# Performance work log

Measured on AMD Instinct MI355X. Metric: run time of the kernel, lower is better.

The kernel has to match this reference:

```python
import jax, jax.numpy as jnp
import numpy as np

N = 60000      # nodes in batch (max_num_cg_nodes_in_batch = 80000)
E = 150000     # edges per edge type
T = 4          # primary edge types (doubled by add_backwards_edges -> 8)
D = 64         # hidden / embedding size
V = 10000      # subtoken vocab
S = 5          # max subtokens per node label
TIMESTEPS = [7, 1]


def setup_inputs() -> dict:
    key = jax.random.key(0)
    ks = jax.random.split(key, 12)
    sc = 1.0 / np.sqrt(D)
    return {
        "node_subtokens": jax.random.randint(ks[0], (N, S), 0, V),
        "adjacency_lists": jax.random.randint(ks[1], (T, E, 2), 0, N),
        "embed_table": jax.random.normal(ks[2], (V, D), jnp.float32) * 0.1,
        "proj_W": jax.random.normal(ks[3], (D, D), jnp.float32) * sc,
        "edge_W0": jax.random.normal(ks[4], (2 * T, D, D), jnp.float32) * sc,
        "edge_W1": jax.random.normal(ks[5], (2 * T, D, D), jnp.float32) * sc,
        "gru0_Wx": jax.random.normal(ks[6], (D, 3 * D), jnp.float32) * sc,
        "gru0_Wh": jax.random.normal(ks[7], (D, 3 * D), jnp.float32) * sc,
        "gru0_b": jnp.zeros((3 * D,), jnp.float32),
        "gru1_Wx": jax.random.normal(ks[8], (2 * D, 3 * D), jnp.float32) * sc,
        "gru1_Wh": jax.random.normal(ks[9], (D, 3 * D), jnp.float32) * sc,
        "gru1_b": jnp.zeros((3 * D,), jnp.float32),
    }


def _gru(x, h, Wx, Wh, b):
    gx = x @ Wx + b          # [N, 3D]
    gh = h @ Wh              # [N, 3D]
    xr, xu, xc = jnp.split(gx, 3, axis=-1)
    hr, hu, hc = jnp.split(gh, 3, axis=-1)
    r = jax.nn.sigmoid(xr + hr)
    u = jax.nn.sigmoid(xu + hu)
    c = jnp.tanh(xc + r * hc)
    return u * h + (1.0 - u) * c


def reference(node_subtokens, adjacency_lists, embed_table, proj_W,
              edge_W0, edge_W1, gru0_Wx, gru0_Wh, gru0_b,
              gru1_Wx, gru1_Wh, gru1_b):
    # Effective edge types: forward + backward (add_backwards_edges=True)
    srcs = jnp.concatenate([adjacency_lists[:, :, 0], adjacency_lists[:, :, 1]], 0)  # [2T, E]
    dsts = jnp.concatenate([adjacency_lists[:, :, 1], adjacency_lists[:, :, 0]], 0)  # [2T, E]
    flat_dsts = dsts.reshape(-1)

    def aggregate(h, edge_W):
        gathered = h[srcs]                                 # [2T, E, D] gather
        msgs = jnp.einsum('ted,tdk->tek', gathered, edge_W)  # per-edge-type transform
        m = jax.ops.segment_max(msgs.reshape(-1, D), flat_dsts, num_segments=N)
        # nodes with no incoming edges get -inf from segment_max -> zero them
        return jnp.where(jnp.isfinite(m), m, 0.0)

    # Subtoken embedding: mean-pool subtoken embeddings, project to hidden
    node_emb = embed_table[node_subtokens].mean(axis=1)    # [N, D]
    h_init = node_emb @ proj_W                             # [N, D]

    # Layer 0: 7 timesteps, no residual
    h = h_init
    for _ in range(TIMESTEPS[0]):
        h = _gru(aggregate(h, edge_W0), h, gru0_Wx, gru0_Wh, gru0_b)

    # Layer 1: 1 timestep, residual from layer index 0 (= initial node states)
    for _ in range(TIMESTEPS[1]):
        msg = aggregate(h, edge_W1)
        h = _gru(jnp.concatenate([h_init, msg], axis=-1), h, gru1_Wx, gru1_Wh, gru1_b)

    return h  # [N, D] final node representations
```

## Files before the change

### kernel.cpp

```cpp
#include <hip/hip_runtime.h>

typedef short v8s __attribute__((ext_vector_type(8)));
typedef float v4f __attribute__((ext_vector_type(4)));

__device__ __forceinline__ unsigned short f2bf(float x) {
  unsigned u = __float_as_uint(x);
  u = u + 0x7FFFu + ((u >> 16) & 1u);
  return (unsigned short)(u >> 16);
}
__device__ __forceinline__ float bf2f(unsigned short b) {
  return __uint_as_float(((unsigned)b) << 16);
}
__device__ __forceinline__ float sigmoidf_(float x) {
  return 1.f / (1.f + __expf(-x));
}
__device__ __forceinline__ float tanhf_(float x) {
  x = fminf(fmaxf(x, -20.f), 20.f);
  float e2 = __expf(2.f * x);
  return (e2 - 1.f) / (e2 + 1.f);
}
__device__ __forceinline__ int swz(int row, int byteInRow) {
  return row * 128 + (byteInRow ^ ((row & 7) << 4));
}

__device__ __forceinline__ void wprep_one(const float* W, unsigned short* O,
                                          int K, int J, int idx) {
  int nkc = K >> 5, nct = J >> 4;
  int j = idx & 7, lane = (idx >> 3) & 63;
  int rest = idx >> 9;
  int ct = rest % nct; rest /= nct;
  int kc = rest % nkc; rest /= nkc;
  int p = rest & 1, t = rest >> 1;
  int row = kc * 32 + (lane >> 4) * 8 + j;
  int col = ct * 16 + (lane & 15);
  float v = W[(size_t)t * K * J + (size_t)row * J + col];
  unsigned short hi = f2bf(v);
  O[idx] = p ? f2bf(v - bf2f(hi)) : hi;
}

__global__ void k_wprep_all(
    const float* eW0, const float* eW1, const float* projW,
    const float* g0Wx, const float* g0Wh, const float* g1Wx, const float* g1Wh,
    unsigned short* eW0f, unsigned short* eW1f, unsigned short* projf,
    unsigned short* g0xf, unsigned short* g0hf,
    unsigned short* g1xf, unsigned short* g1hf) {
  int rel = blockIdx.x * 256 + threadIdx.x;
  if (rel < 65536) { wprep_one(eW0, eW0f, 64, 64, rel); return; }
  rel -= 65536;
  if (rel < 65536) { wprep_one(eW1, eW1f, 64, 64, rel); return; }
  rel -= 65536;
  if (rel < 8192)  { wprep_one(projW, projf, 64, 64, rel); return; }
  rel -= 8192;
  if (rel < 24576) { wprep_one(g0Wx, g0xf, 64, 192, rel); return; }
  rel -= 24576;
  if (rel < 24576) { wprep_one(g0Wh, g0hf, 64, 192, rel); return; }
  rel -= 24576;
  if (rel < 49152) { wprep_one(g1Wx, g1xf, 128, 192, rel); return; }
  rel -= 49152;
  if (rel < 24576) { wprep_one(g1Wh, g1hf, 64, 192, rel); return; }
}

__global__ __launch_bounds__(256) void k_embed(
    const int* __restrict__ toks, const float* __restrict__ embed,
    unsigned short* __restrict__ eh, unsigned short* __restrict__ el, int N) {
  int w = threadIdx.x >> 6, lane = threadIdx.x & 63;
  int n = blockIdx.x * 4 + w;
  if (n >= N) return;
  float acc = 0.f;
#pragma unroll
  for (int s = 0; s < 5; ++s)
    acc += embed[(size_t)toks[n * 5 + s] * 64 + lane];
  float v = acc * 0.2f;
  unsigned short h = f2bf(v);
  eh[(size_t)n * 64 + lane] = h;
  el[(size_t)n * 64 + lane] = f2bf(v - bf2f(h));
}

__global__ void k_counts(const int* __restrict__ adj, int* __restrict__ counts, int E) {
  int e = blockIdx.x * 256 + threadIdx.x;
  if (e >= E) return;
  int t4 = blockIdx.y;
  int2 ab = *(const int2*)&adj[(size_t)(t4 * E + e) * 2];
  atomicAdd(&counts[ab.y], 1);
  atomicAdd(&counts[ab.x], 1);
}

__global__ __launch_bounds__(1024) void k_scan(const int* __restrict__ counts,
                                               int* __restrict__ offsets,
                                               int* __restrict__ cursor, int n) {
  __shared__ int part[1024];
  int tid = threadIdx.x;
  int chunk = (((n + 1023) >> 10) + 3) & ~3;
  int begin = tid * chunk;
  int end = min(begin + chunk, n);
  int s = 0;
  int i = begin;
  for (; i + 4 <= end; i += 4) {
    int4 v = *(const int4*)&counts[i];
    s += v.x + v.y + v.z + v.w;
  }
  for (; i < end; ++i) s += counts[i];
  part[tid] = s;
  __syncthreads();
  for (int off = 1; off < 1024; off <<= 1) {
    int v = (tid >= off) ? part[tid - off] : 0;
    __syncthreads();
    part[tid] += v;
    __syncthreads();
  }
  int run = part[tid] - s;
  i = begin;
  for (; i + 4 <= end; i += 4) {
    int4 c = *(const int4*)&counts[i];
    int4 o;
    o.x = run; o.y = run + c.x; o.z = o.y + c.y; o.w = o.z + c.z;
    *(int4*)&offsets[i] = o;
    *(int4*)&cursor[i] = o;
    run = o.w + c.w;
  }
  for (; i < end; ++i) {
    offsets[i] = run; cursor[i] = run; run += counts[i];
  }
  if (tid == 1023) offsets[n] = part[1023];
}

__global__ void k_fill(const int* __restrict__ adj, int* __restrict__ cursor,
                       int* __restrict__ entries, int E, int N) {
  int e = blockIdx.x * 256 + threadIdx.x;
  if (e >= E) return;
  int t4 = blockIdx.y;
  int2 ab = *(const int2*)&adj[(size_t)(t4 * E + e) * 2];
  int p1 = atomicAdd(&cursor[ab.y], 1);
  entries[p1] = t4 * N + ab.x;
  int p2 = atomicAdd(&cursor[ab.x], 1);
  entries[p2] = (t4 + 4) * N + ab.y;
}

__global__ __launch_bounds__(256) void k_proj(
    const unsigned short* __restrict__ A0h, const unsigned short* __restrict__ A0l,
    const unsigned short* __restrict__ Wf,
    unsigned short* __restrict__ h_hi, unsigned short* __restrict__ h_lo,
    unsigned short* __restrict__ hinit_b, int N) {
  int tid = threadIdx.x;
  int wv = tid >> 6, lane = tid & 63;
  int lr = lane & 15, lg = lane >> 4;
  int m0 = blockIdx.x * 128 + wv * 32;
  v4f acc[2][4] = {};
#pragma unroll
  for (int kc = 0; kc < 2; ++kc) {
    v8s ah[2], al[2];
#pragma unroll
    for (int mt = 0; mt < 2; ++mt) {
      int row = min(m0 + mt * 16 + lr, N - 1);
      size_t off = (size_t)row * 64 + kc * 32 + lg * 8;
      ah[mt] = *(const v8s*)&A0h[off];
      al[mt] = *(const v8s*)&A0l[off];
    }
#pragma unroll
    for (int ct = 0; ct < 4; ++ct) {
      v8s bh = *(const v8s*)&Wf[((size_t)(kc * 4 + ct)) * 512 + lane * 8];
      v8s bl = *(const v8s*)&Wf[((size_t)((2 + kc) * 4 + ct)) * 512 + lane * 8];
#pragma unroll
      for (int mt = 0; mt < 2; ++mt) {
        acc[mt][ct] = __builtin_amdgcn_mfma_f32_16x16x32_bf16(ah[mt], bh, acc[mt][ct], 0, 0, 0);
        acc[mt][ct] = __builtin_amdgcn_mfma_f32_16x16x32_bf16(al[mt], bh, acc[mt][ct], 0, 0, 0);
        acc[mt][ct] = __builtin_amdgcn_mfma_f32_16x16x32_bf16(ah[mt], bl, acc[mt][ct], 0, 0, 0);
      }
    }
  }
#pragma unroll
  for (int ct = 0; ct < 4; ++ct)
#pragma unroll
    for (int mt = 0; mt < 2; ++mt)
#pragma unroll
      for (int r = 0; r < 4; ++r) {
        int m = m0 + mt * 16 + lg * 4 + r;
        if (m >= N) continue;
        int col = ct * 16 + lr;
        float v = acc[mt][ct][r];
        unsigned short hb = f2bf(v);
        h_hi[(size_t)m * 64 + col] = hb;
        h_lo[(size_t)m * 64 + col] = f2bf(v - bf2f(hb));
        hinit_b[(size_t)m * 64 + col] = hb;
      }
}

__global__ __launch_bounds__(256) void k_mm_t(
    const unsigned short* __restrict__ A0h, const unsigned short* __restrict__ A0l,
    const unsigned short* __restrict__ Wf, unsigned short* __restrict__ C16,
    int N) {
  int tid = threadIdx.x;
  int wv = tid >> 6, lane = tid & 63;
  int lr = lane & 15, lg = lane >> 4;
  int y = blockIdx.y;
  const unsigned short* W0 = Wf + (size_t)y * 8192;
  const unsigned short* W1 = Wf + (size_t)(y + 4) * 8192;
  unsigned short* C0 = C16 + (size_t)y * N * 64;
  unsigned short* C1 = C16 + (size_t)(y + 4) * N * 64;
  int m0 = blockIdx.x * 128 + wv * 32;
  v4f acc0[2][4] = {}, acc1[2][4] = {};
#pragma unroll
  for (int kc = 0; kc < 2; ++kc) {
    v8s ah[2], al[2];
#pragma unroll
    for (int mt = 0; mt < 2; ++mt) {
      int row = min(m0 + mt * 16 + lr, N - 1);
      size_t off = (size_t)row * 64 + kc * 32 + lg * 8;
      ah[mt] = *(const v8s*)&A0h[off];
      al[mt] = *(const v8s*)&A0l[off];
    }
#pragma unroll
    for (int ct = 0; ct < 4; ++ct) {
      v8s bh0 = *(const v8s*)&W0[((size_t)(kc * 4 + ct)) * 512 + lane * 8];
      v8s bl0 = *(const v8s*)&W0[((size_t)((2 + kc) * 4 + ct)) * 512 + lane * 8];
      v8s bh1 = *(const v8s*)&W1[((size_t)(kc * 4 + ct)) * 512 + lane * 8];
      v8s bl1 = *(const v8s*)&W1[((size_t)((2 + kc) * 4 + ct)) * 512 + lane * 8];
#pragma unroll
      for (int mt = 0; mt < 2; ++mt) {
        acc0[mt][ct] = __builtin_amdgcn_mfma_f32_16x16x32_bf16(ah[mt], bh0, acc0[mt][ct], 0, 0, 0);
        acc0[mt][ct] = __builtin_amdgcn_mfma_f32_16x16x32_bf16(al[mt], bh0, acc0[mt][ct], 0, 0, 0);
        acc0[mt][ct] = __builtin_amdgcn_mfma_f32_16x16x32_bf16(ah[mt], bl0, acc0[mt][ct], 0, 0, 0);
        acc1[mt][ct] = __builtin_amdgcn_mfma_f32_16x16x32_bf16(ah[mt], bh1, acc1[mt][ct], 0, 0, 0);
        acc1[mt][ct] = __builtin_amdgcn_mfma_f32_16x16x32_bf16(al[mt], bh1, acc1[mt][ct], 0, 0, 0);
        acc1[mt][ct] = __builtin_amdgcn_mfma_f32_16x16x32_bf16(ah[mt], bl1, acc1[mt][ct], 0, 0, 0);
      }
    }
  }
#pragma unroll
  for (int ct = 0; ct < 4; ++ct)
#pragma unroll
    for (int mt = 0; mt < 2; ++mt)
#pragma unroll
      for (int r = 0; r < 4; ++r) {
        int m = m0 + mt * 16 + lg * 4 + r;
        if (m < N) {
          C0[(size_t)m * 64 + ct * 16 + lr] = f2bf(acc0[mt][ct][r]);
          C1[(size_t)m * 64 + ct * 16 + lr] = f2bf(acc1[mt][ct][r]);
        }
      }
}

template <int FINAL>
__global__ __launch_bounds__(256) void k_iter(
    const unsigned short* __restrict__ HtR, const int* __restrict__ offsets,
    const int* __restrict__ entries,
    unsigned short* __restrict__ hh, unsigned short* __restrict__ hl,
    const unsigned short* __restrict__ hinit_b,
    const unsigned short* __restrict__ Wxf, const unsigned short* __restrict__ Whf,
    const float* __restrict__ bias, const unsigned short* __restrict__ eWf,
    unsigned short* __restrict__ HtW, float* __restrict__ outF, int N) {
  __shared__ __align__(16) char lds_msg[128 * 128];
  __shared__ __align__(16) char lds_hs[FINAL ? 16 : 2 * 128 * 128];
  int tid = threadIdx.x;
  int wv = tid >> 6, lane = tid & 63;
  int lr = lane & 15, lg = lane >> 4;
  int lbase = wv * 32;
  int m0 = blockIdx.x * 128 + lbase;

  int g = lane >> 4, q = lane & 15;
  for (int i32 = 0; i32 < 32; ++i32) {
    int n = min(m0 + i32, N - 1);
    int beg = offsets[n], end = offsets[n + 1];
    float a0 = -3.4e38f, a1 = a0, a2 = a0, a3 = a0;
    float b0 = a0, b1 = a0, b2 = a0, b3 = a0;
    int i = beg;
    for (; i + 8 <= end; i += 8) {
      int eA = entries[i + g];
      int eB = entries[i + 4 + g];
      ushort4 va = *(const ushort4*)&HtR[(size_t)eA * 64 + q * 4];
      ushort4 vb = *(const ushort4*)&HtR[(size_t)eB * 64 + q * 4];
      a0 = fmaxf(a0, bf2f(va.x)); a1 = fmaxf(a1, bf2f(va.y));
      a2 = fmaxf(a2, bf2f(va.z)); a3 = fmaxf(a3, bf2f(va.w));
      b0 = fmaxf(b0, bf2f(vb.x)); b1 = fmaxf(b1, bf2f(vb.y));
      b2 = fmaxf(b2, bf2f(vb.z)); b3 = fmaxf(b3, bf2f(vb.w));
    }
    for (; i < end; i += 4) {
      int idx = min(i + g, end - 1);
      int e = entries[idx];
      ushort4 va = *(const ushort4*)&HtR[(size_t)e * 64 + q * 4];
      a0 = fmaxf(a0, bf2f(va.x)); a1 = fmaxf(a1, bf2f(va.y));
      a2 = fmaxf(a2, bf2f(va.z)); a3 = fmaxf(a3, bf2f(va.w));
    }
    a0 = fmaxf(a0, b0); a1 = fmaxf(a1, b1); a2 = fmaxf(a2, b2); a3 = fmaxf(a3, b3);
    a0 = fmaxf(a0, __shfl_xor(a0, 16)); a1 = fmaxf(a1, __shfl_xor(a1, 16));
    a2 = fmaxf(a2, __shfl_xor(a2, 16)); a3 = fmaxf(a3, __shfl_xor(a3, 16));
    a0 = fmaxf(a0, __shfl_xor(a0, 32)); a1 = fmaxf(a1, __shfl_xor(a1, 32));
    a2 = fmaxf(a2, __shfl_xor(a2, 32)); a3 = fmaxf(a3, __shfl_xor(a3, 32));
    if (g == 0) {
      ushort4 o;
      if (end > beg) {
        o.x = f2bf(a0); o.y = f2bf(a1); o.z = f2bf(a2); o.w = f2bf(a3);
      } else {
        o.x = 0; o.y = 0; o.z = 0; o.w = 0;
      }
      int row = lbase + i32;
      *(ushort4*)(lds_msg + swz(row, q * 8)) = o;
    }
  }

  const int NKCX = FINAL ? 4 : 2;
  v4f acc[2][12] = {};
  v4f acch[2][4] = {};
#pragma unroll
  for (int kc = 0; kc < NKCX; ++kc) {
    int kcl = kc & 1;
    v8s ax[2];
#pragma unroll
    for (int mt = 0; mt < 2; ++mt) {
      if (FINAL && kc < 2) {
        int row = min(m0 + mt * 16 + lr, N - 1);
        ax[mt] = *(const v8s*)&hinit_b[(size_t)row * 64 + kcl * 32 + lg * 8];
      } else {
        int row = lbase + mt * 16 + lr;
        ax[mt] = *(const v8s*)(lds_msg + swz(row, kcl * 64 + lg * 16));
      }
    }
#pragma unroll
    for (int ct = 0; ct < 12; ++ct) {
      v8s bh = *(const v8s*)&Wxf[((size_t)(kc * 12 + ct)) * 512 + lane * 8];
      v8s bl = *(const v8s*)&Wxf[((size_t)((NKCX + kc) * 12 + ct)) * 512 + lane * 8];
#pragma unroll
      for (int mt = 0; mt < 2; ++mt) {
        acc[mt][ct] = __builtin_amdgcn_mfma_f32_16x16x32_bf16(ax[mt], bh, acc[mt][ct], 0, 0, 0);
        acc[mt][ct] = __builtin_amdgcn_mfma_f32_16x16x32_bf16(ax[mt], bl, acc[mt][ct], 0, 0, 0);
      }
    }
  }
#pragma unroll
  for (int kc = 0; kc < 2; ++kc) {
    v8s ah[2], al[2];
#pragma unroll
    for (int mt = 0; mt < 2; ++mt) {
      int row = min(m0 + mt * 16 + lr, N - 1);
      size_t off = (size_t)row * 64 + kc * 32 + lg * 8;
      ah[mt] = *(const v8s*)&hh[off];
      al[mt] = *(const v8s*)&hl[off];
    }
#pragma unroll
    for (int ct = 0; ct < 12; ++ct) {
      v8s bh = *(const v8s*)&Whf[((size_t)(kc * 12 + ct)) * 512 + lane * 8];
      v8s bl = *(const v8s*)&Whf[((size_t)((2 + kc) * 12 + ct)) * 512 + lane * 8];
#pragma unroll
      for (int mt = 0; mt < 2; ++mt) {
        v4f* d = (ct < 8) ? &acc[mt][ct] : &acch[mt][ct - 8];
        *d = __builtin_amdgcn_mfma_f32_16x16x32_bf16(ah[mt], bh, *d, 0, 0, 0);
        *d = __builtin_amdgcn_mfma_f32_16x16x32_bf16(al[mt], bh, *d, 0, 0, 0);
        *d = __builtin_amdgcn_mfma_f32_16x16x32_bf16(ah[mt], bl, *d, 0, 0, 0);
      }
    }
  }
#pragma unroll
  for (int mt = 0; mt < 2; ++mt)
#pragma unroll
    for (int ctg = 0; ctg < 4; ++ctg)
#pragma unroll
      for (int r = 0; r < 4; ++r) {
        int m = m0 + mt * 16 + lg * 4 + r;
        int col = ctg * 16 + lr;
        unsigned short hbv = hh[(size_t)min(m, N - 1) * 64 + col];
        unsigned short hlv = hl[(size_t)min(m, N - 1) * 64 + col];
        float hv = bf2f(hbv) + bf2f(hlv);
        float rr = sigmoidf_(acc[mt][ctg][r] + bias[col]);
        float uu = sigmoidf_(acc[mt][ctg + 4][r] + bias[64 + col]);
        float cc = tanhf_(acc[mt][ctg + 8][r] + bias[128 + col] + rr * acch[mt][ctg][r]);
        float ho = uu * hv + (1.f - uu) * cc;
        if (FINAL) {
          if (m < N) outF[(size_t)m * 64 + col] = ho;
        } else {
          unsigned short ohi = f2bf(ho);
          unsigned short olo = f2bf(ho - bf2f(ohi));
          if (m < N) {
            hh[(size_t)m * 64 + col] = ohi;
            hl[(size_t)m * 64 + col] = olo;
          }
          int row = lbase + mt * 16 + lg * 4 + r;
          *(unsigned short*)(lds_hs + swz(row, col * 2)) = ohi;
          *(unsigned short*)(lds_hs + 128 * 128 + swz(row, col * 2)) = olo;
        }
      }

  if (FINAL) return;

  v8s tah[2][2], tal[2][2];
#pragma unroll
  for (int kc = 0; kc < 2; ++kc)
#pragma unroll
    for (int mt = 0; mt < 2; ++mt) {
      int row = lbase + mt * 16 + lr;
      tah[kc][mt] = *(const v8s*)(lds_hs + swz(row, kc * 64 + lg * 16));
      tal[kc][mt] = *(const v8s*)(lds_hs + 128 * 128 + swz(row, kc * 64 + lg * 16));
    }
#pragma unroll
  for (int y = 0; y < 4; ++y) {
    const unsigned short* W0 = eWf + (size_t)y * 8192;
    const unsigned short* W1 = eWf + (size_t)(y + 4) * 8192;
    unsigned short* C0 = HtW + (size_t)y * N * 64;
    unsigned short* C1 = HtW + (size_t)(y + 4) * N * 64;
    v4f acc0[2][4] = {}, acc1[2][4] = {};
#pragma unroll
    for (int kc = 0; kc < 2; ++kc)
#pragma unroll
      for (int ct = 0; ct < 4; ++ct) {
        v8s bh0 = *(const v8s*)&W0[((size_t)(kc * 4 + ct)) * 512 + lane * 8];
        v8s bl0 = *(const v8s*)&W0[((size_t)((2 + kc) * 4 + ct)) * 512 + lane * 8];
        v8s bh1 = *(const v8s*)&W1[((size_t)(kc * 4 + ct)) * 512 + lane * 8];
        v8s bl1 = *(const v8s*)&W1[((size_t)((2 + kc) * 4 + ct)) * 512 + lane * 8];
#pragma unroll
        for (int mt = 0; mt < 2; ++mt) {
          acc0[mt][ct] = __builtin_amdgcn_mfma_f32_16x16x32_bf16(tah[kc][mt], bh0, acc0[mt][ct], 0, 0, 0);
          acc0[mt][ct] = __builtin_amdgcn_mfma_f32_16x16x32_bf16(tal[kc][mt], bh0, acc0[mt][ct], 0, 0, 0);
          acc0[mt][ct] = __builtin_amdgcn_mfma_f32_16x16x32_bf16(tah[kc][mt], bl0, acc0[mt][ct], 0, 0, 0);
          acc1[mt][ct] = __builtin_amdgcn_mfma_f32_16x16x32_bf16(tah[kc][mt], bh1, acc1[mt][ct], 0, 0, 0);
          acc1[mt][ct] = __builtin_amdgcn_mfma_f32_16x16x32_bf16(tal[kc][mt], bh1, acc1[mt][ct], 0, 0, 0);
          acc1[mt][ct] = __builtin_amdgcn_mfma_f32_16x16x32_bf16(tah[kc][mt], bl1, acc1[mt][ct], 0, 0, 0);
        }
      }
#pragma unroll
    for (int ct = 0; ct < 4; ++ct)
#pragma unroll
      for (int mt = 0; mt < 2; ++mt)
#pragma unroll
        for (int r = 0; r < 4; ++r) {
          int m = m0 + mt * 16 + lg * 4 + r;
          if (m < N) {
            C0[(size_t)m * 64 + ct * 16 + lr] = f2bf(acc0[mt][ct][r]);
            C1[(size_t)m * 64 + ct * 16 + lr] = f2bf(acc1[mt][ct][r]);
          }
        }
  }
}

extern "C" void kernel_launch(void* const* d_in, const int* in_sizes, int n_in,
                              void* d_out, int out_size, void* d_ws, size_t ws_size,
                              hipStream_t stream) {
  const int*   toks  = (const int*)d_in[0];
  const int*   adj   = (const int*)d_in[1];
  const float* embed = (const float*)d_in[2];
  const float* projW = (const float*)d_in[3];
  const float* eW0   = (const float*)d_in[4];
  const float* eW1   = (const float*)d_in[5];
  const float* g0Wx  = (const float*)d_in[6];
  const float* g0Wh  = (const float*)d_in[7];
  const float* g0b   = (const float*)d_in[8];
  const float* g1Wx  = (const float*)d_in[9];
  const float* g1Wh  = (const float*)d_in[10];
  const float* g1b   = (const float*)d_in[11];
  float* out = (float*)d_out;

  int N = in_sizes[0] / 5;
  int E = in_sizes[1] / 8;
  size_t ND = (size_t)N * 64;

  char* p = (char*)d_ws;
  unsigned short* Ht0     = (unsigned short*)p; p += 8 * ND * 2;
  unsigned short* Ht1     = (unsigned short*)p; p += 8 * ND * 2;
  unsigned short* h_hi    = (unsigned short*)p; p += ND * 2;
  unsigned short* h_lo    = (unsigned short*)p; p += ND * 2;
  unsigned short* hinit_b = (unsigned short*)p; p += ND * 2;
  int* offsets = (int*)p; p += (size_t)(N + 64) * sizeof(int);
  int* cnt_cur = (int*)p; p += (size_t)(N + 64) * sizeof(int);
  int* entries = (int*)p; p += (size_t)8 * E * sizeof(int);
  unsigned short* eW0f  = (unsigned short*)p; p += 65536 * 2;
  unsigned short* eW1f  = (unsigned short*)p; p += 65536 * 2;
  unsigned short* projf = (unsigned short*)p; p += 8192 * 2;
  unsigned short* g0xf  = (unsigned short*)p; p += 24576 * 2;
  unsigned short* g0hf  = (unsigned short*)p; p += 24576 * 2;
  unsigned short* g1xf  = (unsigned short*)p; p += 49152 * 2;
  unsigned short* g1hf  = (unsigned short*)p; p += 24576 * 2;
  if ((size_t)(p - (char*)d_ws) > ws_size) return;

  unsigned short* emb_h = Ht0;
  unsigned short* emb_l = Ht0 + ND;

  int g128 = (N + 127) / 128;
  int g4 = (N + 3) / 4;

  k_wprep_all<<<1024, 256, 0, stream>>>(eW0, eW1, projW, g0Wx, g0Wh, g1Wx, g1Wh,
                                        eW0f, eW1f, projf, g0xf, g0hf, g1xf, g1hf);
  hipMemsetAsync(cnt_cur, 0, (size_t)N * sizeof(int), stream);
  dim3 egrid((E + 255) / 256, 4);
  k_counts<<<egrid, 256, 0, stream>>>(adj, cnt_cur, E);
  k_embed<<<g4, 256, 0, stream>>>(toks, embed, emb_h, emb_l, N);
  k_proj<<<g128, 256, 0, stream>>>(emb_h, emb_l, projf, h_hi, h_lo, hinit_b, N);
  k_scan<<<1, 1024, 0, stream>>>(cnt_cur, offsets, cnt_cur, N);
  k_fill<<<egrid, 256, 0, stream>>>(adj, cnt_cur, entries, E, N);
  k_mm_t<<<dim3(g128, 4), 256, 0, stream>>>(h_hi, h_lo, eW0f, Ht0, N);

  unsigned short* bufs[2] = {Ht0, Ht1};
  for (int it = 0; it < 7; ++it) {
    unsigned short* HtR = bufs[it & 1];
    unsigned short* HtW = bufs[(it + 1) & 1];
    const unsigned short* ef = (it < 6) ? eW0f : eW1f;
    k_iter<0><<<g128, 256, 0, stream>>>(HtR, offsets, entries, h_hi, h_lo,
                                        hinit_b, g0xf, g0hf, g0b, ef,
                                        HtW, nullptr, N);
  }
  k_iter<1><<<g128, 256, 0, stream>>>(bufs[1], offsets, entries, h_hi, h_lo,
                                      hinit_b, g1xf, g1hf, g1b, nullptr,
                                      nullptr, out, N);
}
```

Measured before the change: 1.226 ms.

## Split fused gather-max from GRU/transform kernel into separate aggregation kernel

The edge gather and segment-max now live in their own kernel, with one wavefront per node across many small blocks, instead of each wave serially walking 32 nodes inside the fused GRU kernel. The max results go to a global bf16 buffer that the GRU/transform kernel reads directly. This raises the parallelism and latency hiding of the irregular gather, and lets the GEMM kernel drop its message LDS buffer. Because the two phases are now separate launches, the transformed table can be updated in place, so the double-buffered table becomes a single buffer. The costs are an extra global write and read of the message array and one more launch per step.

```diff
diff --git a/kernel.cpp b/kernel.cpp
--- a/kernel.cpp
+++ b/kernel.cpp
@@ -240,16 +240,57 @@
       }
 }
 
+__global__ __launch_bounds__(256) void k_aggmax(
+    const unsigned short* __restrict__ Htb, const int* __restrict__ offsets,
+    const int* __restrict__ entries, unsigned short* __restrict__ mh, int N) {
+  int w = threadIdx.x >> 6, lane = threadIdx.x & 63;
+  int n = blockIdx.x * 4 + w;
+  if (n >= N) return;
+  int beg = offsets[n], end = offsets[n + 1];
+  int g = lane >> 4, q = lane & 15;
+  float a0 = -3.4e38f, a1 = a0, a2 = a0, a3 = a0;
+  float b0 = a0, b1 = a0, b2 = a0, b3 = a0;
+  int i = beg;
+  for (; i + 8 <= end; i += 8) {
+    int eA = entries[i + g];
+    int eB = entries[i + 4 + g];
+    ushort4 va = *(const ushort4*)&Htb[(size_t)eA * 64 + q * 4];
+    ushort4 vb = *(const ushort4*)&Htb[(size_t)eB * 64 + q * 4];
+    a0 = fmaxf(a0, bf2f(va.x)); a1 = fmaxf(a1, bf2f(va.y));
+    a2 = fmaxf(a2, bf2f(va.z)); a3 = fmaxf(a3, bf2f(va.w));
+    b0 = fmaxf(b0, bf2f(vb.x)); b1 = fmaxf(b1, bf2f(vb.y));
+    b2 = fmaxf(b2, bf2f(vb.z)); b3 = fmaxf(b3, bf2f(vb.w));
+  }
+  for (; i < end; i += 4) {
+    int idx = min(i + g, end - 1);
+    int e = entries[idx];
+    ushort4 va = *(const ushort4*)&Htb[(size_t)e * 64 + q * 4];
+    a0 = fmaxf(a0, bf2f(va.x)); a1 = fmaxf(a1, bf2f(va.y));
+    a2 = fmaxf(a2, bf2f(va.z)); a3 = fmaxf(a3, bf2f(va.w));
+  }
+  a0 = fmaxf(a0, b0); a1 = fmaxf(a1, b1); a2 = fmaxf(a2, b2); a3 = fmaxf(a3, b3);
+  a0 = fmaxf(a0, __shfl_xor(a0, 16)); a1 = fmaxf(a1, __shfl_xor(a1, 16));
+  a2 = fmaxf(a2, __shfl_xor(a2, 16)); a3 = fmaxf(a3, __shfl_xor(a3, 16));
+  a0 = fmaxf(a0, __shfl_xor(a0, 32)); a1 = fmaxf(a1, __shfl_xor(a1, 32));
+  a2 = fmaxf(a2, __shfl_xor(a2, 32)); a3 = fmaxf(a3, __shfl_xor(a3, 32));
+  if (g == 0) {
+    ushort4 o;
+    if (end > beg) {
+      o.x = f2bf(a0); o.y = f2bf(a1); o.z = f2bf(a2); o.w = f2bf(a3);
+    } else {
+      o.x = 0; o.y = 0; o.z = 0; o.w = 0;
+    }
+    *(ushort4*)&mh[(size_t)n * 64 + q * 4] = o;
+  }
+}
+
 template <int FINAL>
-__global__ __launch_bounds__(256) void k_iter(
-    const unsigned short* __restrict__ HtR, const int* __restrict__ offsets,
-    const int* __restrict__ entries,
+__global__ __launch_bounds__(256) void k_gt(
+    const unsigned short* __restrict__ x0, const unsigned short* __restrict__ x1,
     unsigned short* __restrict__ hh, unsigned short* __restrict__ hl,
-    const unsigned short* __restrict__ hinit_b,
     const unsigned short* __restrict__ Wxf, const unsigned short* __restrict__ Whf,
     const float* __restrict__ bias, const unsigned short* __restrict__ eWf,
     unsigned short* __restrict__ HtW, float* __restrict__ outF, int N) {
-  __shared__ __align__(16) char lds_msg[128 * 128];
   __shared__ __align__(16) char lds_hs[FINAL ? 16 : 2 * 128 * 128];
   int tid = threadIdx.x;
   int wv = tid >> 6, lane = tid & 63;
@@ -257,63 +298,18 @@
   int lbase = wv * 32;
   int m0 = blockIdx.x * 128 + lbase;
 
-  int g = lane >> 4, q = lane & 15;
-  for (int i32 = 0; i32 < 32; ++i32) {
-    int n = min(m0 + i32, N - 1);
-    int beg = offsets[n], end = offsets[n + 1];
-    float a0 = -3.4e38f, a1 = a0, a2 = a0, a3 = a0;
-    float b0 = a0, b1 = a0, b2 = a0, b3 = a0;
-    int i = beg;
-    for (; i + 8 <= end; i += 8) {
-      int eA = entries[i + g];
-      int eB = entries[i + 4 + g];
-      ushort4 va = *(const ushort4*)&HtR[(size_t)eA * 64 + q * 4];
-      ushort4 vb = *(const ushort4*)&HtR[(size_t)eB * 64 + q * 4];
-      a0 = fmaxf(a0, bf2f(va.x)); a1 = fmaxf(a1, bf2f(va.y));
-      a2 = fmaxf(a2, bf2f(va.z)); a3 = fmaxf(a3, bf2f(va.w));
-      b0 = fmaxf(b0, bf2f(vb.x)); b1 = fmaxf(b1, bf2f(vb.y));
-      b2 = fmaxf(b2, bf2f(vb.z)); b3 = fmaxf(b3, bf2f(vb.w));
-    }
-    for (; i < end; i += 4) {
-      int idx = min(i + g, end - 1);
-      int e = entries[idx];
-      ushort4 va = *(const ushort4*)&HtR[(size_t)e * 64 + q * 4];
-      a0 = fmaxf(a0, bf2f(va.x)); a1 = fmaxf(a1, bf2f(va.y));
-      a2 = fmaxf(a2, bf2f(va.z)); a3 = fmaxf(a3, bf2f(va.w));
-    }
-    a0 = fmaxf(a0, b0); a1 = fmaxf(a1, b1); a2 = fmaxf(a2, b2); a3 = fmaxf(a3, b3);
-    a0 = fmaxf(a0, __shfl_xor(a0, 16)); a1 = fmaxf(a1, __shfl_xor(a1, 16));
-    a2 = fmaxf(a2, __shfl_xor(a2, 16)); a3 = fmaxf(a3, __shfl_xor(a3, 16));
-    a0 = fmaxf(a0, __shfl_xor(a0, 32)); a1 = fmaxf(a1, __shfl_xor(a1, 32));
-    a2 = fmaxf(a2, __shfl_xor(a2, 32)); a3 = fmaxf(a3, __shfl_xor(a3, 32));
-    if (g == 0) {
-      ushort4 o;
-      if (end > beg) {
-        o.x = f2bf(a0); o.y = f2bf(a1); o.z = f2bf(a2); o.w = f2bf(a3);
-      } else {
-        o.x = 0; o.y = 0; o.z = 0; o.w = 0;
-      }
-      int row = lbase + i32;
-      *(ushort4*)(lds_msg + swz(row, q * 8)) = o;
-    }
-  }
-
   const int NKCX = FINAL ? 4 : 2;
   v4f acc[2][12] = {};
   v4f acch[2][4] = {};
 #pragma unroll
   for (int kc = 0; kc < NKCX; ++kc) {
+    const unsigned short* X = (FINAL && kc >= 2) ? x1 : x0;
     int kcl = kc & 1;
     v8s ax[2];
 #pragma unroll
     for (int mt = 0; mt < 2; ++mt) {
-      if (FINAL && kc < 2) {
-        int row = min(m0 + mt * 16 + lr, N - 1);
-        ax[mt] = *(const v8s*)&hinit_b[(size_t)row * 64 + kcl * 32 + lg * 8];
-      } else {
-        int row = lbase + mt * 16 + lr;
-        ax[mt] = *(const v8s*)(lds_msg + swz(row, kcl * 64 + lg * 16));
-      }
+      int row = min(m0 + mt * 16 + lr, N - 1);
+      ax[mt] = *(const v8s*)&X[(size_t)row * 64 + kcl * 32 + lg * 8];
     }
 #pragma unroll
     for (int ct = 0; ct < 12; ++ct) {
@@ -452,11 +448,11 @@
   size_t ND = (size_t)N * 64;
 
   char* p = (char*)d_ws;
-  unsigned short* Ht0     = (unsigned short*)p; p += 8 * ND * 2;
-  unsigned short* Ht1     = (unsigned short*)p; p += 8 * ND * 2;
+  unsigned short* Htb     = (unsigned short*)p; p += 8 * ND * 2;
   unsigned short* h_hi    = (unsigned short*)p; p += ND * 2;
   unsigned short* h_lo    = (unsigned short*)p; p += ND * 2;
   unsigned short* hinit_b = (unsigned short*)p; p += ND * 2;
+  unsigned short* m_hi    = (unsigned short*)p; p += ND * 2;
   int* offsets = (int*)p; p += (size_t)(N + 64) * sizeof(int);
   int* cnt_cur = (int*)p; p += (size_t)(N + 64) * sizeof(int);
   int* entries = (int*)p; p += (size_t)8 * E * sizeof(int);
@@ -469,8 +465,8 @@
   unsigned short* g1hf  = (unsigned short*)p; p += 24576 * 2;
   if ((size_t)(p - (char*)d_ws) > ws_size) return;
 
-  unsigned short* emb_h = Ht0;
-  unsigned short* emb_l = Ht0 + ND;
+  unsigned short* emb_h = Htb;
+  unsigned short* emb_l = Htb + ND;
 
   int g128 = (N + 127) / 128;
   int g4 = (N + 3) / 4;
@@ -484,18 +480,15 @@
   k_proj<<<g128, 256, 0, stream>>>(emb_h, emb_l, projf, h_hi, h_lo, hinit_b, N);
   k_scan<<<1, 1024, 0, stream>>>(cnt_cur, offsets, cnt_cur, N);
   k_fill<<<egrid, 256, 0, stream>>>(adj, cnt_cur, entries, E, N);
-  k_mm_t<<<dim3(g128, 4), 256, 0, stream>>>(h_hi, h_lo, eW0f, Ht0, N);
-
-  unsigned short* bufs[2] = {Ht0, Ht1};
+  k_mm_t<<<dim3(g128, 4), 256, 0, stream>>>(h_hi, h_lo, eW0f, Htb, N);
+
   for (int it = 0; it < 7; ++it) {
-    unsigned short* HtR = bufs[it & 1];
-    unsigned short* HtW = bufs[(it + 1) & 1];
+    k_aggmax<<<g4, 256, 0, stream>>>(Htb, offsets, entries, m_hi, N);
     const unsigned short* ef = (it < 6) ? eW0f : eW1f;
-    k_iter<0><<<g128, 256, 0, stream>>>(HtR, offsets, entries, h_hi, h_lo,
-                                        hinit_b, g0xf, g0hf, g0b, ef,
-                                        HtW, nullptr, N);
-  }
-  k_iter<1><<<g128, 256, 0, stream>>>(bufs[1], offsets, entries, h_hi, h_lo,
-                                      hinit_b, g1xf, g1hf, g1b, nullptr,
-                                      nullptr, out, N);
-}
+    k_gt<0><<<g128, 256, 0, stream>>>(m_hi, nullptr, h_hi, h_lo,
+                                      g0xf, g0hf, g0b, ef, Htb, nullptr, N);
+  }
+  k_aggmax<<<g4, 256, 0, stream>>>(Htb, offsets, entries, m_hi, N);
+  k_gt<1><<<g128, 256, 0, stream>>>(hinit_b, m_hi, h_hi, h_lo,
+                                    g1xf, g1hf, g1b, nullptr, nullptr, out, N);
+}
```

After: 1.113 ms. -9.2%, faster.
